# Kernel optimization log

Measured on AMD Instinct MI355X. Metric: run time of the kernel, lower is better.

## Reference

```python
import jax, jax.numpy as jnp
import numpy as np

B, S, D = 4, 2048, 1024
H, DH = 16, 64  # d_model = H*DH = 1024
NEG = 1e10


def setup_inputs() -> dict:
    key = jax.random.key(0)
    ks = jax.random.split(key, 5)
    scale = 1.0 / np.sqrt(D)
    x = jax.random.normal(ks[0], (B, S, D), dtype=jnp.float32)
    mask = jax.random.randint(ks[1], (B, S), 0, 2).astype(jnp.float32)
    Wq = jax.random.normal(ks[2], (D, H * DH), dtype=jnp.float32) * scale
    Wk = jax.random.normal(ks[3], (D, H * DH), dtype=jnp.float32) * scale
    Wv = jax.random.normal(ks[4], (D, H * DH), dtype=jnp.float32) * scale
    z = jnp.zeros((H * DH,), dtype=jnp.float32)
    return {"x": x, "mask": mask, "Wq": Wq, "bq": z, "Wk": Wk, "bk": z,
            "Wv": Wv, "bv": z}


def reference(x, mask, Wq, bq, Wk, bk, Wv, bv):
    # projections -> [B, H, S, DH]
    def proj(W, b):
        y = x @ W + b
        return y.reshape(B, S, H, DH).transpose(0, 2, 1, 3)

    q, k, v = proj(Wq, bq), proj(Wk, bk), proj(Wv, bv)
    scores = jnp.einsum("bhsd,bhtd->bhst", q, k) / np.sqrt(DH)
    m = mask[:, None, None, :]                      # [B,1,1,S]
    scores = scores - (1.0 - m) * NEG               # additive mask
    probs = jax.nn.softmax(scores, axis=-1)         # stable (max-subtract)
    probs = probs * m                               # multiplicative mask
    out = jnp.einsum("bhst,bhtd->bhsd", probs, v)   # [B,H,S,DH]
    return out.transpose(0, 2, 1, 3).reshape(B, S, H * DH)
```

## Files before the change

### kernel.cpp

```cpp
#include <hip/hip_runtime.h>

typedef float f32x4 __attribute__((ext_vector_type(4)));
typedef float f32x16 __attribute__((ext_vector_type(16)));
typedef _Float16 f16;
typedef _Float16 f16x2 __attribute__((ext_vector_type(2)));
typedef _Float16 f16x8 __attribute__((ext_vector_type(8)));
typedef unsigned int u32x2 __attribute__((ext_vector_type(2)));
typedef unsigned short u16;
typedef unsigned short u16x4 __attribute__((ext_vector_type(4)));
typedef unsigned int u32;

#define S_LEN 2048
#define NHEAD 16
#define DHEAD 64
#define DMODEL 1024
#define NBATCH 4

__device__ __forceinline__ void gload16(const u16* g, const uint4* l) {
  __builtin_amdgcn_global_load_lds((const __attribute__((address_space(1))) void*)g,
                                   (__attribute__((address_space(3))) void*)l, 16, 0, 0);
}


__global__ void cvt_x(const float* __restrict__ x, u16* __restrict__ o, int n4) {
  int i = blockIdx.x * blockDim.x + threadIdx.x;
  int st = gridDim.x * blockDim.x;
  for (; i < n4; i += st) {
    float4 v = reinterpret_cast<const float4*>(x)[i];
    uint2 r;
    r.x = __builtin_bit_cast(u32, __builtin_amdgcn_cvt_pkrtz(v.x, v.y));
    r.y = __builtin_bit_cast(u32, __builtin_amdgcn_cvt_pkrtz(v.z, v.w));
    reinterpret_cast<uint2*>(o)[i] = r;
  }
}

__global__ void trans_w(const float* __restrict__ W, u16* __restrict__ wt) {
  __shared__ float t[32][33];
  int bx = blockIdx.x * 32, by = blockIdx.y * 32;
  int tx = threadIdx.x & 31, ty = threadIdx.x >> 5;
#pragma unroll
  for (int i = 0; i < 32; i += 8)
    t[ty + i][tx] = W[(size_t)(by + ty + i) * DMODEL + bx + tx];
  __syncthreads();
#pragma unroll
  for (int i = 0; i < 32; i += 8)
    wt[(size_t)(bx + ty + i) * DMODEL + by + tx] = __builtin_bit_cast(u16, (f16)t[tx][ty + i]);
}

__global__ __launch_bounds__(512, 2) void qkv_gemm(
    const u16* __restrict__ A, const u16* __restrict__ Wt,
    const float* __restrict__ bq, const float* __restrict__ bk, const float* __restrict__ bv,
    const float* __restrict__ mask,
    u16* __restrict__ Qo, u16* __restrict__ Ko, u16* __restrict__ Vo)
{
  __shared__ uint4 As4[4][1024];
  __shared__ uint4 Bs4[4][1024];
  const int tid = threadIdx.x;
  const int lane = tid & 63;
  const int wid = tid >> 6;
  const int l31 = lane & 31, hi = lane >> 5;

  const int id = blockIdx.x;
  const int swz = (id & 7) * 48 + (id >> 3);
  const int m0 = (swz & 31) * 256;
  const int n0 = (swz >> 5) * 256;

  const int wrM = (wid >> 2) * 128;
  const int wcN = (wid & 3) * 64;

  f32x16 acc[4][2] = {};

  const int r0 = tid >> 2;
  const int r1 = r0 + 128;
  const int p4 = tid & 3;
  const int sl0 = p4 ^ ((r0 >> 1) & 3);
  const int sl1 = p4 ^ ((r1 >> 1) & 3);
  const u16* ag0 = A  + (size_t)(m0 + r0) * 1024 + sl0 * 8;
  const u16* ag1 = A  + (size_t)(m0 + r1) * 1024 + sl1 * 8;
  const u16* bg0 = Wt + (size_t)(n0 + r0) * 1024 + sl0 * 8;
  const u16* bg1 = Wt + (size_t)(n0 + r1) * 1024 + sl1 * 8;

  auto stage = [&](int buf, int kt) {
    gload16(ag0 + kt * 32, &As4[buf][wid * 64]);
    gload16(ag1 + kt * 32, &As4[buf][wid * 64 + 512]);
    gload16(bg0 + kt * 32, &Bs4[buf][wid * 64]);
    gload16(bg1 + kt * 32, &Bs4[buf][wid * 64 + 512]);
  };

  int aoff[4][2], boff[2][2];
#pragma unroll
  for (int mi = 0; mi < 4; mi++) {
    int r = wrM + mi * 32 + l31;
#pragma unroll
    for (int ks = 0; ks < 2; ks++)
      aoff[mi][ks] = r * 32 + (((ks * 2 + hi) ^ ((r >> 1) & 3)) * 8);
  }
#pragma unroll
  for (int ni = 0; ni < 2; ni++) {
    int r = wcN + ni * 32 + l31;
#pragma unroll
    for (int ks = 0; ks < 2; ks++)
      boff[ni][ks] = r * 32 + (((ks * 2 + hi) ^ ((r >> 1) & 3)) * 8);
  }

  stage(0, 0);
  stage(1, 1);
  stage(2, 2);
  __syncthreads();

  const int NT = 1024 / 32;
  for (int it = 0; it < NT; ++it) {
    if (it + 2 < NT)      asm volatile("s_waitcnt vmcnt(8)" ::: "memory");
    else if (it + 1 < NT) asm volatile("s_waitcnt vmcnt(4)" ::: "memory");
    else                  asm volatile("s_waitcnt vmcnt(0)" ::: "memory");
    __builtin_amdgcn_s_barrier();
    __builtin_amdgcn_sched_barrier(0);
    const int cur = it & 3;
    if (it + 3 < NT) stage((it + 3) & 3, it + 3);

    const u16* As = (const u16*)&As4[cur][0];
    const u16* Bs = (const u16*)&Bs4[cur][0];
    f16x8 af[4][2], bf[2][2];
#pragma unroll
    for (int mi = 0; mi < 4; mi++)
#pragma unroll
      for (int ks = 0; ks < 2; ks++)
        af[mi][ks] = *(const f16x8*)&As[aoff[mi][ks]];
#pragma unroll
    for (int ni = 0; ni < 2; ni++)
#pragma unroll
      for (int ks = 0; ks < 2; ks++)
        bf[ni][ks] = *(const f16x8*)&Bs[boff[ni][ks]];

#pragma unroll
    for (int ks = 0; ks < 2; ks++)
#pragma unroll
      for (int mi = 0; mi < 4; mi++)
#pragma unroll
        for (int ni = 0; ni < 2; ni++)
          acc[mi][ni] = __builtin_amdgcn_mfma_f32_32x32x16_f16(af[mi][ks], bf[ni][ks], acc[mi][ni], 0, 0, 0);
  }

  const int sel = n0 >> 10;
  const float* bias = (sel == 0) ? bq : (sel == 1) ? bk : bv;
  const int nb = (n0 & 1023) + wcN;
  const float QSCALE = 0.18033688011112042f;
#pragma unroll
  for (int mi = 0; mi < 4; mi++)
#pragma unroll
    for (int ni = 0; ni < 2; ni++) {
      const int ncol = nb + ni * 32 + l31;
      const float bi = bias[ncol];
      const int h = ncol >> 6, dh = ncol & 63;
#pragma unroll
      for (int r4 = 0; r4 < 4; r4++) {
        const int rowb = m0 + wrM + mi * 32 + 8 * r4 + 4 * hi;
        const int bb = rowb >> 11, s0 = rowb & 2047;
        const size_t bh = (size_t)(bb * NHEAD + h);
        if (sel == 0) {
#pragma unroll
          for (int j = 0; j < 4; j++)
            Qo[(bh * S_LEN + s0 + j) * DHEAD + dh] =
                __builtin_bit_cast(u16, (f16)((acc[mi][ni][r4 * 4 + j] + bi) * QSCALE));
        } else if (sel == 1) {
#pragma unroll
          for (int j = 0; j < 4; j++)
            Ko[(bh * S_LEN + s0 + j) * DHEAD + dh] =
                __builtin_bit_cast(u16, (f16)(acc[mi][ni][r4 * 4 + j] + bi));
        } else {
          u16x4 pk;
#pragma unroll
          for (int j = 0; j < 4; j++) {
            float v = acc[mi][ni][r4 * 4 + j] + bi;
            if (mask[bb * S_LEN + s0 + j] <= 0.f) v = 0.f;
            pk[j] = __builtin_bit_cast(u16, (f16)v);
          }
          *(u16x4*)&Vo[(bh * DHEAD + dh) * S_LEN + s0] = pk;
        }
      }
    }
}

__global__ __launch_bounds__(256, 2) void attn(
    const u16* __restrict__ Q, const u16* __restrict__ K, const u16* __restrict__ Vt,
    const float* __restrict__ mask, float* __restrict__ out)
{
  __shared__ uint4 Ks4[3][512];
  __shared__ uint4 Vs4[3][512];
  __shared__ __align__(16) u16 MsAll[S_LEN];
  const int tid = threadIdx.x;
  const int lane = tid & 63, wid = tid >> 6;
  const int l31 = lane & 31, hi = lane >> 5;
  const int sid = blockIdx.x;
  const int qt = (sid >> 3) & 7;
  const int bh = (sid & 7) + 8 * (sid >> 6);
  const int b = bh >> 4, h = bh & 15;
  const size_t base = (size_t)bh * S_LEN * DHEAD;
  const u16* Qp = Q + base;
  const u16* Kp = K + base;
  const u16* Vp = Vt + base;
  const float* mp = mask + b * S_LEN;
  const int q0 = qt * 256 + wid * 64;

  f16x8 aqA[4], aqB[4];
#pragma unroll
  for (int kc = 0; kc < 4; kc++) {
    aqA[kc] = *(const f16x8*)&Qp[(size_t)(q0 + l31) * DHEAD + kc * 16 + hi * 8];
    aqB[kc] = *(const f16x8*)&Qp[(size_t)(q0 + 32 + l31) * DHEAD + kc * 16 + hi * 8];
  }

  f32x16 accO0A = {}, accO1A = {}, accLA = {};
  f32x16 accO0B = {}, accO1B = {}, accLB = {};

  const int cA_ = wid * 128 + lane, cB_ = cA_ + 64;
  const int rk0 = cA_ >> 3, rk1 = cB_ >> 3;
  const int p8 = lane & 7;
  const int cc0 = (p8 - ((rk0 + (rk0 >> 3)) & 7)) & 7;
  const int cc1 = (p8 - ((rk1 + (rk1 >> 3)) & 7)) & 7;
  const u16* kg0 = Kp + (size_t)rk0 * DHEAD + cc0 * 8;
  const u16* kg1 = Kp + (size_t)rk1 * DHEAD + cc1 * 8;
  const u16* vg0 = Vp + (size_t)rk0 * S_LEN + cc0 * 8;
  const u16* vg1 = Vp + (size_t)rk1 * S_LEN + cc1 * 8;

  auto stage = [&](int buf) {
    gload16(kg0, &Ks4[buf][wid * 128]); gload16(kg1, &Ks4[buf][wid * 128 + 64]);
    gload16(vg0, &Vs4[buf][wid * 128]); gload16(vg1, &Vs4[buf][wid * 128 + 64]);
    kg0 += 64 * DHEAD; kg1 += 64 * DHEAD; vg0 += 64; vg1 += 64;
  };

  const int swA = (l31 + (l31 >> 3)) & 7;
  const int swB = (swA + 4) & 7;
  int idxA[4], idxB[4];
#pragma unroll
  for (int kc = 0; kc < 4; kc++) {
    idxA[kc] = l31 * 8 + ((kc * 2 + hi + swA) & 7);
    idxB[kc] = (32 + l31) * 8 + ((kc * 2 + hi + swB) & 7);
  }

  {
    float4 ml0 = *(const float4*)&mp[tid * 8];
    float4 ml1 = *(const float4*)&mp[tid * 8 + 4];
    uint4 w;
    w.x = __builtin_bit_cast(u32, __builtin_amdgcn_cvt_pkrtz(ml0.x, ml0.y));
    w.y = __builtin_bit_cast(u32, __builtin_amdgcn_cvt_pkrtz(ml0.z, ml0.w));
    w.z = __builtin_bit_cast(u32, __builtin_amdgcn_cvt_pkrtz(ml1.x, ml1.y));
    w.w = __builtin_bit_cast(u32, __builtin_amdgcn_cvt_pkrtz(ml1.z, ml1.w));
    *(uint4*)&MsAll[tid * 8] = w;
  }
  stage(0);
  stage(1);
  __syncthreads();

  const int NT = S_LEN / 64;
  for (int it = 0; it < NT; ++it) {
    if (it + 1 < NT) asm volatile("s_waitcnt vmcnt(4)" ::: "memory");
    else             asm volatile("s_waitcnt vmcnt(0)" ::: "memory");
    __builtin_amdgcn_s_barrier();
    __builtin_amdgcn_sched_barrier(0);
    const int cur = it % 3;
    const uint4* ks = &Ks4[cur][0];
    const uint4* vs = &Vs4[cur][0];
    if (it + 2 < NT) stage((it + 2) % 3);

    f32x16 sA0 = {}, sA1 = {}, sB0 = {}, sB1 = {};
#pragma unroll
    for (int kc = 0; kc < 4; kc++) {
      f16x8 k0 = *(const f16x8*)&ks[idxA[kc]];
      f16x8 k1 = *(const f16x8*)&ks[idxB[kc]];
      sA0 = __builtin_amdgcn_mfma_f32_32x32x16_f16(k0, aqA[kc], sA0, 0, 0, 0);
      sA1 = __builtin_amdgcn_mfma_f32_32x32x16_f16(k1, aqA[kc], sA1, 0, 0, 0);
      sB0 = __builtin_amdgcn_mfma_f32_32x32x16_f16(k0, aqB[kc], sB0, 0, 0, 0);
      sB1 = __builtin_amdgcn_mfma_f32_32x32x16_f16(k1, aqB[kc], sB1, 0, 0, 0);
    }

#pragma unroll
    for (int g = 0; g < 4; g++) {
      const f32x16& srcA = (g < 2) ? sA0 : sA1;
      const f32x16& srcB = (g < 2) ? sB0 : sB1;
      const int o = (g & 1) * 8;
      u32 wa[4], wb[4];
#pragma unroll
      for (int s = 0; s < 4; s++) {
        wa[s] = __builtin_bit_cast(u32, __builtin_amdgcn_cvt_pkrtz(
                    __builtin_amdgcn_exp2f(srcA[o + 2 * s]),
                    __builtin_amdgcn_exp2f(srcA[o + 2 * s + 1])));
        wb[s] = __builtin_bit_cast(u32, __builtin_amdgcn_cvt_pkrtz(
                    __builtin_amdgcn_exp2f(srcB[o + 2 * s]),
                    __builtin_amdgcn_exp2f(srcB[o + 2 * s + 1])));
      }
      u32x2 rA0 = __builtin_amdgcn_permlane32_swap(wa[0], wa[2], false, false);
      u32x2 rA1 = __builtin_amdgcn_permlane32_swap(wa[1], wa[3], false, false);
      u32x2 rB0 = __builtin_amdgcn_permlane32_swap(wb[0], wb[2], false, false);
      u32x2 rB1 = __builtin_amdgcn_permlane32_swap(wb[1], wb[3], false, false);
      uint4 f4A; f4A.x = rA0[0]; f4A.y = rA1[0]; f4A.z = rA0[1]; f4A.w = rA1[1];
      uint4 f4B; f4B.x = rB0[0]; f4B.y = rB1[0]; f4B.z = rB0[1]; f4B.w = rB1[1];
      f16x8 fA = __builtin_bit_cast(f16x8, f4A);
      f16x8 fB = __builtin_bit_cast(f16x8, f4B);
      f16x8 bv0 = *(const f16x8*)&vs[idxA[g]];
      f16x8 bv1 = *(const f16x8*)&vs[idxB[g]];
      f16x8 bm = *(const f16x8*)&MsAll[it * 64 + g * 16 + hi * 8];
      accO0A = __builtin_amdgcn_mfma_f32_32x32x16_f16(fA, bv0, accO0A, 0, 0, 0);
      accO1A = __builtin_amdgcn_mfma_f32_32x32x16_f16(fA, bv1, accO1A, 0, 0, 0);
      accLA  = __builtin_amdgcn_mfma_f32_32x32x16_f16(fA, bm,  accLA,  0, 0, 0);
      accO0B = __builtin_amdgcn_mfma_f32_32x32x16_f16(fB, bv0, accO0B, 0, 0, 0);
      accO1B = __builtin_amdgcn_mfma_f32_32x32x16_f16(fB, bv1, accO1B, 0, 0, 0);
      accLB  = __builtin_amdgcn_mfma_f32_32x32x16_f16(fB, bm,  accLB,  0, 0, 0);
    }
  }

#pragma unroll
  for (int r = 0; r < 16; r++) {
    int qr = (r & 3) + 8 * (r >> 2) + 4 * hi;
    float lA = accLA[r], lB = accLB[r];
    float iA = (lA > 0.f) ? 1.f / lA : 0.f;
    float iB = (lB > 0.f) ? 1.f / lB : 0.f;
    float* opA = out + ((size_t)(b * S_LEN + q0 + qr) * DMODEL) + h * DHEAD;
    float* opB = out + ((size_t)(b * S_LEN + q0 + 32 + qr) * DMODEL) + h * DHEAD;
    opA[l31] = accO0A[r] * iA;
    opA[32 + l31] = accO1A[r] * iA;
    opB[l31] = accO0B[r] * iB;
    opB[32 + l31] = accO1B[r] * iB;
  }
}

extern "C" void kernel_launch(void* const* d_in, const int* in_sizes, int n_in,
                              void* d_out, int out_size, void* d_ws, size_t ws_size,
                              hipStream_t stream) {
  const float* x    = (const float*)d_in[0];
  const float* mask = (const float*)d_in[1];
  const float* Wq   = (const float*)d_in[2];
  const float* bq   = (const float*)d_in[3];
  const float* Wk   = (const float*)d_in[4];
  const float* bk   = (const float*)d_in[5];
  const float* Wv   = (const float*)d_in[6];
  const float* bv   = (const float*)d_in[7];
  float* out = (float*)d_out;

  u16* xb = (u16*)d_ws;
  u16* wt = xb + (size_t)8192 * 1024;
  u16* Qb = wt + (size_t)3072 * 1024;
  u16* Kb = Qb + (size_t)8388608;
  u16* Vb = Kb + (size_t)8388608;

  cvt_x<<<2048, 256, 0, stream>>>(x, xb, (8192 * 1024) / 4);
  trans_w<<<dim3(32, 32), 256, 0, stream>>>(Wq, wt);
  trans_w<<<dim3(32, 32), 256, 0, stream>>>(Wk, wt + (size_t)1024 * 1024);
  trans_w<<<dim3(32, 32), 256, 0, stream>>>(Wv, wt + (size_t)2 * 1024 * 1024);
  qkv_gemm<<<dim3(384), 512, 0, stream>>>(xb, wt, bq, bk, bv, mask, Qb, Kb, Vb);
  attn<<<512, 256, 0, stream>>>(Qb, Kb, Vb, mask, out);
}
```

Before: 190.2 us.

## Shrink QKV GEMM tiles to 128x128, add MFMA priority hints in attention

The QKV GEMM moves from 256x256 tiles with 512 threads and a 4-stage LDS pipeline to 128x128 tiles with 256 threads, a 3-stage pipeline and a 2D grid without block swizzling. The V epilogue loads the mask as a float4 instead of four scalar loads. The attention kernel wraps its MFMA sections in s_setprio so waves issuing matrix work are favoured by the scheduler. Smaller GEMM tiles give more blocks and less LDS per block, but they also cut data reuse and drop the L2-friendly swizzle.

```diff
diff --git a/kernel.cpp b/kernel.cpp
--- a/kernel.cpp
+++ b/kernel.cpp
@@ -47,32 +47,27 @@
     wt[(size_t)(bx + ty + i) * DMODEL + by + tx] = __builtin_bit_cast(u16, (f16)t[tx][ty + i]);
 }
 
-__global__ __launch_bounds__(512, 2) void qkv_gemm(
+__global__ __launch_bounds__(256) void qkv_gemm(
     const u16* __restrict__ A, const u16* __restrict__ Wt,
     const float* __restrict__ bq, const float* __restrict__ bk, const float* __restrict__ bv,
     const float* __restrict__ mask,
     u16* __restrict__ Qo, u16* __restrict__ Ko, u16* __restrict__ Vo)
 {
-  __shared__ uint4 As4[4][1024];
-  __shared__ uint4 Bs4[4][1024];
+  __shared__ uint4 As4[3][512];
+  __shared__ uint4 Bs4[3][512];
   const int tid = threadIdx.x;
   const int lane = tid & 63;
   const int wid = tid >> 6;
   const int l31 = lane & 31, hi = lane >> 5;
-
-  const int id = blockIdx.x;
-  const int swz = (id & 7) * 48 + (id >> 3);
-  const int m0 = (swz & 31) * 256;
-  const int n0 = (swz >> 5) * 256;
-
-  const int wrM = (wid >> 2) * 128;
-  const int wcN = (wid & 3) * 64;
-
-  f32x16 acc[4][2] = {};
-
-  const int r0 = tid >> 2;
-  const int r1 = r0 + 128;
-  const int p4 = tid & 3;
+  const int m0 = blockIdx.x * 128;
+  const int n0 = blockIdx.y * 128;
+  const int wr = (wid >> 1) * 64, wc = (wid & 1) * 64;
+
+  f32x16 acc[2][2] = {};
+
+  const int c0 = wid * 64 + lane, c1 = c0 + 256;
+  const int r0 = c0 >> 2, r1 = c1 >> 2;
+  const int p4 = lane & 3;
   const int sl0 = p4 ^ ((r0 >> 1) & 3);
   const int sl1 = p4 ^ ((r1 >> 1) & 3);
   const u16* ag0 = A  + (size_t)(m0 + r0) * 1024 + sl0 * 8;
@@ -81,48 +76,46 @@
   const u16* bg1 = Wt + (size_t)(n0 + r1) * 1024 + sl1 * 8;
 
   auto stage = [&](int buf, int kt) {
-    gload16(ag0 + kt * 32, &As4[buf][wid * 64]);
-    gload16(ag1 + kt * 32, &As4[buf][wid * 64 + 512]);
-    gload16(bg0 + kt * 32, &Bs4[buf][wid * 64]);
-    gload16(bg1 + kt * 32, &Bs4[buf][wid * 64 + 512]);
+    gload16(ag0 + kt, &As4[buf][wid * 64]);
+    gload16(ag1 + kt, &As4[buf][wid * 64 + 256]);
+    gload16(bg0 + kt, &Bs4[buf][wid * 64]);
+    gload16(bg1 + kt, &Bs4[buf][wid * 64 + 256]);
   };
 
-  int aoff[4][2], boff[2][2];
-#pragma unroll
-  for (int mi = 0; mi < 4; mi++) {
-    int r = wrM + mi * 32 + l31;
+  int aoff[2][2], boff[2][2];
+#pragma unroll
+  for (int mi = 0; mi < 2; mi++) {
+    int r = wr + mi * 32 + l31;
 #pragma unroll
     for (int ks = 0; ks < 2; ks++)
       aoff[mi][ks] = r * 32 + (((ks * 2 + hi) ^ ((r >> 1) & 3)) * 8);
   }
 #pragma unroll
   for (int ni = 0; ni < 2; ni++) {
-    int r = wcN + ni * 32 + l31;
+    int r = wc + ni * 32 + l31;
 #pragma unroll
     for (int ks = 0; ks < 2; ks++)
       boff[ni][ks] = r * 32 + (((ks * 2 + hi) ^ ((r >> 1) & 3)) * 8);
   }
 
   stage(0, 0);
-  stage(1, 1);
-  stage(2, 2);
+  stage(1, 32);
   __syncthreads();
 
   const int NT = 1024 / 32;
   for (int it = 0; it < NT; ++it) {
-    if (it + 2 < NT)      asm volatile("s_waitcnt vmcnt(8)" ::: "memory");
-    else if (it + 1 < NT) asm volatile("s_waitcnt vmcnt(4)" ::: "memory");
-    else                  asm volatile("s_waitcnt vmcnt(0)" ::: "memory");
+    if (it + 1 < NT) asm volatile("s_waitcnt vmcnt(4)" ::: "memory");
+    else             asm volatile("s_waitcnt vmcnt(0)" ::: "memory");
     __builtin_amdgcn_s_barrier();
     __builtin_amdgcn_sched_barrier(0);
-    const int cur = it & 3;
-    if (it + 3 < NT) stage((it + 3) & 3, it + 3);
+    const int cur = it % 3;
+    if (it + 2 < NT) stage((it + 2) % 3, (it + 2) * 32);
 
     const u16* As = (const u16*)&As4[cur][0];
     const u16* Bs = (const u16*)&Bs4[cur][0];
-    f16x8 af[4][2], bf[2][2];
-#pragma unroll
-    for (int mi = 0; mi < 4; mi++)
+    f16x8 af[2][2], bf[2][2];
+#pragma unroll
+    for (int mi = 0; mi < 2; mi++)
 #pragma unroll
       for (int ks = 0; ks < 2; ks++)
         af[mi][ks] = *(const f16x8*)&As[aoff[mi][ks]];
@@ -135,7 +128,7 @@
 #pragma unroll
     for (int ks = 0; ks < 2; ks++)
 #pragma unroll
-      for (int mi = 0; mi < 4; mi++)
+      for (int mi = 0; mi < 2; mi++)
 #pragma unroll
         for (int ni = 0; ni < 2; ni++)
           acc[mi][ni] = __builtin_amdgcn_mfma_f32_32x32x16_f16(af[mi][ks], bf[ni][ks], acc[mi][ni], 0, 0, 0);
@@ -143,18 +136,18 @@
 
   const int sel = n0 >> 10;
   const float* bias = (sel == 0) ? bq : (sel == 1) ? bk : bv;
-  const int nb = (n0 & 1023) + wcN;
+  const int nbase = (n0 & 1023) + wc;
   const float QSCALE = 0.18033688011112042f;
 #pragma unroll
-  for (int mi = 0; mi < 4; mi++)
+  for (int mi = 0; mi < 2; mi++)
 #pragma unroll
     for (int ni = 0; ni < 2; ni++) {
-      const int ncol = nb + ni * 32 + l31;
+      const int ncol = nbase + ni * 32 + l31;
       const float bi = bias[ncol];
       const int h = ncol >> 6, dh = ncol & 63;
 #pragma unroll
       for (int r4 = 0; r4 < 4; r4++) {
-        const int rowb = m0 + wrM + mi * 32 + 8 * r4 + 4 * hi;
+        const int rowb = m0 + wr + mi * 32 + 8 * r4 + 4 * hi;
         const int bb = rowb >> 11, s0 = rowb & 2047;
         const size_t bh = (size_t)(bb * NHEAD + h);
         if (sel == 0) {
@@ -168,11 +161,13 @@
             Ko[(bh * S_LEN + s0 + j) * DHEAD + dh] =
                 __builtin_bit_cast(u16, (f16)(acc[mi][ni][r4 * 4 + j] + bi));
         } else {
+          const float4 mk = *(const float4*)&mask[bb * S_LEN + s0];
           u16x4 pk;
 #pragma unroll
           for (int j = 0; j < 4; j++) {
             float v = acc[mi][ni][r4 * 4 + j] + bi;
-            if (mask[bb * S_LEN + s0 + j] <= 0.f) v = 0.f;
+            float mj = (j == 0) ? mk.x : (j == 1) ? mk.y : (j == 2) ? mk.z : mk.w;
+            if (mj <= 0.f) v = 0.f;
             pk[j] = __builtin_bit_cast(u16, (f16)v);
           }
           *(u16x4*)&Vo[(bh * DHEAD + dh) * S_LEN + s0] = pk;
@@ -263,6 +258,7 @@
     if (it + 2 < NT) stage((it + 2) % 3);
 
     f32x16 sA0 = {}, sA1 = {}, sB0 = {}, sB1 = {};
+    __builtin_amdgcn_s_setprio(1);
 #pragma unroll
     for (int kc = 0; kc < 4; kc++) {
       f16x8 k0 = *(const f16x8*)&ks[idxA[kc]];
@@ -272,6 +268,7 @@
       sB0 = __builtin_amdgcn_mfma_f32_32x32x16_f16(k0, aqB[kc], sB0, 0, 0, 0);
       sB1 = __builtin_amdgcn_mfma_f32_32x32x16_f16(k1, aqB[kc], sB1, 0, 0, 0);
     }
+    __builtin_amdgcn_s_setprio(0);
 
 #pragma unroll
     for (int g = 0; g < 4; g++) {
@@ -299,12 +296,14 @@
       f16x8 bv0 = *(const f16x8*)&vs[idxA[g]];
       f16x8 bv1 = *(const f16x8*)&vs[idxB[g]];
       f16x8 bm = *(const f16x8*)&MsAll[it * 64 + g * 16 + hi * 8];
+      __builtin_amdgcn_s_setprio(1);
       accO0A = __builtin_amdgcn_mfma_f32_32x32x16_f16(fA, bv0, accO0A, 0, 0, 0);
       accO1A = __builtin_amdgcn_mfma_f32_32x32x16_f16(fA, bv1, accO1A, 0, 0, 0);
       accLA  = __builtin_amdgcn_mfma_f32_32x32x16_f16(fA, bm,  accLA,  0, 0, 0);
       accO0B = __builtin_amdgcn_mfma_f32_32x32x16_f16(fB, bv0, accO0B, 0, 0, 0);
       accO1B = __builtin_amdgcn_mfma_f32_32x32x16_f16(fB, bv1, accO1B, 0, 0, 0);
       accLB  = __builtin_amdgcn_mfma_f32_32x32x16_f16(fB, bm,  accLB,  0, 0, 0);
+      __builtin_amdgcn_s_setprio(0);
     }
   }
 
@@ -346,6 +345,6 @@
   trans_w<<<dim3(32, 32), 256, 0, stream>>>(Wq, wt);
   trans_w<<<dim3(32, 32), 256, 0, stream>>>(Wk, wt + (size_t)1024 * 1024);
   trans_w<<<dim3(32, 32), 256, 0, stream>>>(Wv, wt + (size_t)2 * 1024 * 1024);
-  qkv_gemm<<<dim3(384), 512, 0, stream>>>(xb, wt, bq, bk, bv, mask, Qb, Kb, Vb);
+  qkv_gemm<<<dim3(64, 24), 256, 0, stream>>>(xb, wt, bq, bk, bv, mask, Qb, Kb, Vb);
   attn<<<512, 256, 0, stream>>>(Qb, Kb, Vb, mask, out);
 }
```

Result: faster. 168.7 us (-11.3%).
